# Kernel tuning notes

Measured on AMD Instinct MI355X. Metric: run time of the kernel, lower is better.

## Reference

```python
import jax, jax.numpy as jnp
import numpy as np

IGNORE_INDEX = -100
ALPHA = 1.0
TOPK = 20


def setup_inputs() -> dict:
    key = jax.random.key(0)
    k1, k2 = jax.random.split(key)
    N, V = 4096, 50257
    source = jax.random.normal(k1, (N, V), dtype=jnp.float32)
    target = jax.random.randint(k2, (N,), 0, V, dtype=jnp.int64)
    return {"source": source, "target": target}


def reference(source, target):
    s = source.astype(jnp.float32)  # [N, V]
    valid = target != IGNORE_INDEX  # [N]

    # per-token cross entropy, reduction='none' (0 at ignored positions)
    lse = jax.nn.logsumexp(s, axis=-1)  # [N]
    safe_tgt = jnp.where(valid, target, 0)
    tgt_logit = jnp.take_along_axis(s, safe_tgt[:, None], axis=-1)[:, 0]
    per_token_loss = jnp.where(valid, lse - tgt_logit, 0.0)

    # entropy-based adaptive weight over top-k logits (no grad in original)
    k = min(TOPK, s.shape[-1])
    topk_val, _ = jax.lax.top_k(s, k)  # [N, k]
    log_probs_topk = topk_val - jax.nn.logsumexp(topk_val, axis=-1, keepdims=True)
    entropy_approx = -(jnp.exp(log_probs_topk) * log_probs_topk).sum(axis=-1)
    adaptive_weight = jnp.power(entropy_approx / 3.0, ALPHA)
    adaptive_weight = jnp.where(valid, adaptive_weight, 0.0)
    adaptive_weight = jax.lax.stop_gradient(adaptive_weight)

    # reduction='mean' over valid tokens
    loss = (per_token_loss * adaptive_weight).sum() / valid.sum()
    return loss.astype(source.dtype)
```

## Files before the change

kernel.cpp:

```cpp
#include <hip/hip_runtime.h>
#include <stdint.h>

#define TOPK 20
#define BLK 256
#define CAP 4096
#define DELTA 2.0f
#define LSTRIDE 21
#define L2E 1.4426950408889634f
#define IGNORE_INDEX (-100)

__device__ __forceinline__ unsigned fkey(float x) {
  unsigned b = __float_as_uint(x);
  return (b & 0x80000000u) ? ~b : (b | 0x80000000u);
}
__device__ __forceinline__ float funkey(unsigned k) {
  unsigned b = (k & 0x80000000u) ? (k & 0x7FFFFFFFu) : ~k;
  return __uint_as_float(b);
}

struct LSE { float m; float l; };
__device__ __forceinline__ void lse_up(LSE& s, float x) {
  if (x > s.m) { s.l *= exp2f((s.m - x) * L2E); s.m = x; }
  s.l += exp2f((x - s.m) * L2E);
}

__device__ __forceinline__ void ins20(float (&tv)[TOPK], float c) {
  if (c > tv[TOPK - 1]) {
#pragma unroll
    for (int j = 0; j < TOPK; ++j) {
      float hi = fmaxf(tv[j], c);
      c = fminf(tv[j], c);
      tv[j] = hi;
    }
  }
}

__device__ __forceinline__ void merge2(const float* A, const float* B, float* O) {
  int i = 1, j = 1;
  float a = A[0], b = B[0];
#pragma unroll
  for (int k = 0; k < TOPK; ++k) {
    if (a >= b) { O[k] = a; a = A[i]; ++i; }
    else        { O[k] = b; b = B[j]; ++j; }
  }
}

__device__ float* merge64(int tid, float* bufA, float* bufB) {
  float* srcb = bufA;
  float* dstb = bufB;
  for (int s = 32; s >= 1; s >>= 1) {
    __syncthreads();
    if (tid < s) {
      merge2(srcb + tid * LSTRIDE, srcb + (tid + s) * LSTRIDE, dstb + tid * LSTRIDE);
      dstb[tid * LSTRIDE + TOPK] = -INFINITY;
    }
    float* t = srcb; srcb = dstb; dstb = t;
  }
  __syncthreads();
  return srcb;
}

__global__ __launch_bounds__(BLK) void eaft_ce_kernel(
    const float* __restrict__ src, const int* __restrict__ tgt,
    float* __restrict__ acc, int V) {
  __shared__ float s_cand[CAP];
  __shared__ float s_bufA[64 * LSTRIDE];
  __shared__ float s_bufB[64 * LSTRIDE];
  __shared__ float s_m[BLK];
  __shared__ float s_l[BLK];
  __shared__ unsigned s_maxkey;
  __shared__ int s_cnt;
  __shared__ int s_slow;

  const int tid = threadIdx.x;
  const int row = blockIdx.x;
  if (tid == 0) { s_maxkey = 0u; s_cnt = 0; s_slow = 0; }
  __syncthreads();

  const size_t rowbase = (size_t)row * (size_t)V;
  const float* arow = src + rowbase;
  const int mis = (int)(rowbase & 3);
  const int head = (4 - mis) & 3;
  const float4* vp = (const float4*)(arow + head);
  const int nvec = (V - head) >> 2;
  const int tail = V - head - (nvec << 2);

  LSE st; st.m = -INFINITY; st.l = 0.f;
  float lmax = -INFINITY;

  float4 pv = make_float4(-INFINITY, -INFINITY, -INFINITY, -INFINITY);
  if (tid < nvec) pv = vp[tid];
  float ex = -INFINITY;
  if (tid < head) ex = arow[tid];
  else if (tid >= 64 && tid < 64 + tail) ex = arow[head + (nvec << 2) + (tid - 64)];

  {
    float vals[5] = {pv.x, pv.y, pv.z, pv.w, ex};
#pragma unroll
    for (int q = 0; q < 5; ++q) {
      float x = vals[q];
      if (x != -INFINITY) {
        lse_up(st, x);
        if (x > lmax) { lmax = x; atomicMax(&s_maxkey, fkey(x)); }
      }
    }
  }
  __syncthreads();

  {
    float bm = funkey(*(volatile unsigned*)&s_maxkey);
    if (bm > lmax) lmax = bm;
    float T = bm - DELTA;
    float vals[5] = {pv.x, pv.y, pv.z, pv.w, ex};
#pragma unroll
    for (int q = 0; q < 5; ++q) {
      float x = vals[q];
      if (x >= T) {
        int p = atomicAdd(&s_cnt, 1);
        if (p < CAP) s_cand[p] = x;
      }
    }
  }

  for (int i = BLK + tid; i < nvec; i += BLK) {
    float4 x4 = vp[i];
    unsigned k = *(volatile unsigned*)&s_maxkey;
    float bm = funkey(k);
    if (bm > lmax) lmax = bm;
    float T = bm - DELTA;
    float vv[4] = {x4.x, x4.y, x4.z, x4.w};
#pragma unroll
    for (int q = 0; q < 4; ++q) {
      float x = vv[q];
      lse_up(st, x);
      if (x > lmax) { lmax = x; atomicMax(&s_maxkey, fkey(x)); }
      if (x >= T) {
        int p = atomicAdd(&s_cnt, 1);
        if (p < CAP) s_cand[p] = x;
      }
    }
  }

  s_m[tid] = st.m; s_l[tid] = st.l;
  __syncthreads();
  for (int s = BLK / 2; s > 0; s >>= 1) {
    if (tid < s) {
      float m1 = s_m[tid], l1 = s_l[tid];
      float m2 = s_m[tid + s], l2 = s_l[tid + s];
      float M = fmaxf(m1, m2);
      float w1 = (m1 > -INFINITY) ? l1 * exp2f((m1 - M) * L2E) : 0.f;
      float w2 = (m2 > -INFINITY) ? l2 * exp2f((m2 - M) * L2E) : 0.f;
      s_m[tid] = M; s_l[tid] = w1 + w2;
    }
    __syncthreads();
  }
  const float m_row = s_m[0];
  const float lse_row = m_row + logf(s_l[0]);

  const int cnt_raw = s_cnt;
  const int C = cnt_raw < CAP ? cnt_raw : CAP;
  if (tid < 64) {
    float tv[TOPK];
#pragma unroll
    for (int j = 0; j < TOPK; ++j) tv[j] = -INFINITY;
    for (int i = tid; i < C; i += 64) ins20(tv, s_cand[i]);
#pragma unroll
    for (int j = 0; j < TOPK; ++j) s_bufA[tid * LSTRIDE + j] = tv[j];
    s_bufA[tid * LSTRIDE + TOPK] = -INFINITY;
  }
  float* R = merge64(tid, s_bufA, s_bufB);

  if (tid == 0)
    s_slow = (cnt_raw > CAP || R[TOPK - 1] < m_row - DELTA) ? 1 : 0;
  __syncthreads();

  if (s_slow) {
    float tv[TOPK];
#pragma unroll
    for (int j = 0; j < TOPK; ++j) tv[j] = -INFINITY;
    for (int e = tid; e < V; e += BLK) ins20(tv, arow[e]);
    for (int r = 0; r < 4; ++r) {
      __syncthreads();
      if ((tid >> 6) == r) {
        int lane = tid & 63;
#pragma unroll
        for (int j = 0; j < TOPK; ++j) s_bufA[lane * LSTRIDE + j] = tv[j];
        s_bufA[lane * LSTRIDE + TOPK] = -INFINITY;
      }
      float* Rr = merge64(tid, s_bufA, s_bufB);
      if (tid == 0) {
#pragma unroll
        for (int j = 0; j < TOPK; ++j) s_cand[r * LSTRIDE + j] = Rr[j];
        s_cand[r * LSTRIDE + TOPK] = -INFINITY;
      }
      __syncthreads();
    }
    if (tid == 0) {
      merge2(s_cand + 0 * LSTRIDE, s_cand + 1 * LSTRIDE, s_bufA);
      s_bufA[TOPK] = -INFINITY;
      merge2(s_cand + 2 * LSTRIDE, s_cand + 3 * LSTRIDE, s_bufA + LSTRIDE);
      s_bufA[LSTRIDE + TOPK] = -INFINITY;
      merge2(s_bufA, s_bufA + LSTRIDE, s_bufB);
    }
  }
  __syncthreads();

  if (tid == 0) {
    const float* W = s_slow ? s_bufB : R;
    int t = tgt[row];
    if (t != IGNORE_INDEX) {
      float tl = arow[t];
      float loss = lse_row - tl;
      float m0 = W[0];
      float S1 = 0.f, Sv = 0.f;
#pragma unroll
      for (int k2 = 0; k2 < TOPK; ++k2) {
        float v = W[k2];
        float e = exp2f((v - m0) * L2E);
        S1 += e;
        Sv += v * e;
      }
      float ent = (m0 + logf(S1)) - Sv / S1;
      float w = ent * (1.0f / 3.0f);
      atomicAdd(&acc[0], w * loss);
      atomicAdd(&acc[1], 1.0f);
    }
  }
}

__global__ void finalize_kernel(const float* __restrict__ acc, float* __restrict__ out) {
  out[0] = acc[0] / acc[1];
}

extern "C" void kernel_launch(void* const* d_in, const int* in_sizes, int n_in,
                              void* d_out, int out_size, void* d_ws, size_t ws_size,
                              hipStream_t stream) {
  const float* src = (const float*)d_in[0];
  const int* tgt = (const int*)d_in[1];
  const int NV = in_sizes[0];
  const int n = in_sizes[1];
  const int V = NV / n;
  float* ws = (float*)d_ws;
  hipMemsetAsync(ws, 0, 2 * sizeof(float), stream);
  eaft_ce_kernel<<<n, BLK, 0, stream>>>(src, tgt, ws, V);
  finalize_kernel<<<1, 1, 0, stream>>>(ws, (float*)d_out);
}
```

Before: 1.191 ms.

## Use block-shared max for LSE, wave-shuffle reduction, nontemporal 2x-unrolled loads

Per-thread online-softmax rescaling is replaced by a shared running block max: after the first chunk, each thread accumulates exp(x - bm) and rescales only when the shared max grows. This removes a per-element compare-and-rescale. The shared-memory tree reduction becomes a wave-level shuffle reduction plus a 4-way final combine. The main loop is unrolled 2x with nontemporal vector loads, and the candidate buffer is halved to cut LDS use. Risks are more fallbacks to the slow path when candidates overflow, and cross-thread max-update races that are handled by the rescaling.

New measurement: 1.309 ms. 9.9% more time.

```diff
diff --git a/kernel.cpp b/kernel.cpp
--- a/kernel.cpp
+++ b/kernel.cpp
@@ -3,12 +3,14 @@
 
 #define TOPK 20
 #define BLK 256
-#define CAP 4096
+#define CAP 2048
 #define DELTA 2.0f
 #define LSTRIDE 21
 #define L2E 1.4426950408889634f
 #define IGNORE_INDEX (-100)
 
+typedef float f4v __attribute__((ext_vector_type(4)));
+
 __device__ __forceinline__ unsigned fkey(float x) {
   unsigned b = __float_as_uint(x);
   return (b & 0x80000000u) ? ~b : (b | 0x80000000u);
@@ -16,12 +18,6 @@
 __device__ __forceinline__ float funkey(unsigned k) {
   unsigned b = (k & 0x80000000u) ? (k & 0x7FFFFFFFu) : ~k;
   return __uint_as_float(b);
-}
-
-struct LSE { float m; float l; };
-__device__ __forceinline__ void lse_up(LSE& s, float x) {
-  if (x > s.m) { s.l *= exp2f((s.m - x) * L2E); s.m = x; }
-  s.l += exp2f((x - s.m) * L2E);
 }
 
 __device__ __forceinline__ void ins20(float (&tv)[TOPK], float c) {
@@ -66,8 +62,8 @@
   __shared__ float s_cand[CAP];
   __shared__ float s_bufA[64 * LSTRIDE];
   __shared__ float s_bufB[64 * LSTRIDE];
-  __shared__ float s_m[BLK];
-  __shared__ float s_l[BLK];
+  __shared__ float s_wm[4];
+  __shared__ float s_wl[4];
   __shared__ unsigned s_maxkey;
   __shared__ int s_cnt;
   __shared__ int s_slow;
@@ -79,83 +75,109 @@
 
   const size_t rowbase = (size_t)row * (size_t)V;
   const float* arow = src + rowbase;
-  const int mis = (int)(rowbase & 3);
-  const int head = (4 - mis) & 3;
-  const float4* vp = (const float4*)(arow + head);
+  const int head = (int)((4 - (rowbase & 3)) & 3);
+  const f4v* vp = (const f4v*)(arow + head);
   const int nvec = (V - head) >> 2;
   const int tail = V - head - (nvec << 2);
 
-  LSE st; st.m = -INFINITY; st.l = 0.f;
-  float lmax = -INFINITY;
-
-  float4 pv = make_float4(-INFINITY, -INFINITY, -INFINITY, -INFINITY);
-  if (tid < nvec) pv = vp[tid];
+  f4v pv = {-INFINITY, -INFINITY, -INFINITY, -INFINITY};
+  if (tid < nvec) pv = __builtin_nontemporal_load(vp + tid);
   float ex = -INFINITY;
   if (tid < head) ex = arow[tid];
   else if (tid >= 64 && tid < 64 + tail) ex = arow[head + (nvec << 2) + (tid - 64)];
 
+  float pmax = fmaxf(fmaxf(fmaxf(pv.x, pv.y), fmaxf(pv.z, pv.w)), ex);
+  if (pmax > -INFINITY) atomicMax(&s_maxkey, fkey(pmax));
+  __syncthreads();
+
+  float bm = funkey(s_maxkey);
+  float lmax = bm;
+  float cexp = -bm * L2E;
+  float l0 = 0.f, l1 = 0.f;
+
   {
+    float T = bm - DELTA;
     float vals[5] = {pv.x, pv.y, pv.z, pv.w, ex};
 #pragma unroll
     for (int q = 0; q < 5; ++q) {
       float x = vals[q];
-      if (x != -INFINITY) {
-        lse_up(st, x);
+      l0 += exp2f(fmaf(x, L2E, cexp));
+      if (x >= T) {
+        int p = atomicAdd(&s_cnt, 1);
+        if (p < CAP) s_cand[p] = x;
         if (x > lmax) { lmax = x; atomicMax(&s_maxkey, fkey(x)); }
       }
     }
   }
-  __syncthreads();
+
+  int i = BLK + tid;
+  for (; i + BLK < nvec; i += 2 * BLK) {
+    f4v a = __builtin_nontemporal_load(vp + i);
+    f4v b = __builtin_nontemporal_load(vp + i + BLK);
+    float nb = funkey(*(volatile unsigned*)&s_maxkey);
+    if (nb > bm) {
+      float r = exp2f((bm - nb) * L2E);
+      l0 *= r; l1 *= r;
+      bm = nb; cexp = -bm * L2E;
+      if (nb > lmax) lmax = nb;
+    }
+    float T = bm - DELTA;
+    float av[4] = {a.x, a.y, a.z, a.w};
+    float bv[4] = {b.x, b.y, b.z, b.w};
+#pragma unroll
+    for (int q = 0; q < 4; ++q) {
+      float x = av[q];
+      l0 += exp2f(fmaf(x, L2E, cexp));
+      if (x >= T) {
+        int p = atomicAdd(&s_cnt, 1);
+        if (p < CAP) s_cand[p] = x;
+        if (x > lmax) { lmax = x; atomicMax(&s_maxkey, fkey(x)); }
+      }
+      float y = bv[q];
+      l1 += exp2f(fmaf(y, L2E, cexp));
+      if (y >= T) {
+        int p = atomicAdd(&s_cnt, 1);
+        if (p < CAP) s_cand[p] = y;
+        if (y > lmax) { lmax = y; atomicMax(&s_maxkey, fkey(y)); }
+      }
+    }
+  }
+  if (i < nvec) {
+    f4v a = __builtin_nontemporal_load(vp + i);
+    float nb = funkey(*(volatile unsigned*)&s_maxkey);
+    if (nb > bm) {
+      float r = exp2f((bm - nb) * L2E);
+      l0 *= r; l1 *= r;
+      bm = nb; cexp = -bm * L2E;
+      if (nb > lmax) lmax = nb;
+    }
+    float T = bm - DELTA;
+    float av[4] = {a.x, a.y, a.z, a.w};
+#pragma unroll
+    for (int q = 0; q < 4; ++q) {
+      float x = av[q];
+      l0 += exp2f(fmaf(x, L2E, cexp));
+      if (x >= T) {
+        int p = atomicAdd(&s_cnt, 1);
+        if (p < CAP) s_cand[p] = x;
+        if (x > lmax) { lmax = x; atomicMax(&s_maxkey, fkey(x)); }
+      }
+    }
+  }
 
   {
-    float bm = funkey(*(volatile unsigned*)&s_maxkey);
-    if (bm > lmax) lmax = bm;
-    float T = bm - DELTA;
-    float vals[5] = {pv.x, pv.y, pv.z, pv.w, ex};
-#pragma unroll
-    for (int q = 0; q < 5; ++q) {
-      float x = vals[q];
-      if (x >= T) {
-        int p = atomicAdd(&s_cnt, 1);
-        if (p < CAP) s_cand[p] = x;
-      }
-    }
-  }
-
-  for (int i = BLK + tid; i < nvec; i += BLK) {
-    float4 x4 = vp[i];
-    unsigned k = *(volatile unsigned*)&s_maxkey;
-    float bm = funkey(k);
-    if (bm > lmax) lmax = bm;
-    float T = bm - DELTA;
-    float vv[4] = {x4.x, x4.y, x4.z, x4.w};
-#pragma unroll
-    for (int q = 0; q < 4; ++q) {
-      float x = vv[q];
-      lse_up(st, x);
-      if (x > lmax) { lmax = x; atomicMax(&s_maxkey, fkey(x)); }
-      if (x >= T) {
-        int p = atomicAdd(&s_cnt, 1);
-        if (p < CAP) s_cand[p] = x;
-      }
-    }
-  }
-
-  s_m[tid] = st.m; s_l[tid] = st.l;
-  __syncthreads();
-  for (int s = BLK / 2; s > 0; s >>= 1) {
-    if (tid < s) {
-      float m1 = s_m[tid], l1 = s_l[tid];
-      float m2 = s_m[tid + s], l2 = s_l[tid + s];
-      float M = fmaxf(m1, m2);
-      float w1 = (m1 > -INFINITY) ? l1 * exp2f((m1 - M) * L2E) : 0.f;
-      float w2 = (m2 > -INFINITY) ? l2 * exp2f((m2 - M) * L2E) : 0.f;
-      s_m[tid] = M; s_l[tid] = w1 + w2;
-    }
-    __syncthreads();
-  }
-  const float m_row = s_m[0];
-  const float lse_row = m_row + logf(s_l[0]);
+    float m = bm, l = l0 + l1;
+#pragma unroll
+    for (int off = 32; off > 0; off >>= 1) {
+      float om = __shfl_down(m, off);
+      float ol = __shfl_down(l, off);
+      float M = fmaxf(m, om);
+      l = l * exp2f((m - M) * L2E) + ol * exp2f((om - M) * L2E);
+      m = M;
+    }
+    if ((tid & 63) == 0) { s_wm[tid >> 6] = m; s_wl[tid >> 6] = l; }
+  }
+  __syncthreads();
 
   const int cnt_raw = s_cnt;
   const int C = cnt_raw < CAP ? cnt_raw : CAP;
@@ -163,15 +185,16 @@
     float tv[TOPK];
 #pragma unroll
     for (int j = 0; j < TOPK; ++j) tv[j] = -INFINITY;
-    for (int i = tid; i < C; i += 64) ins20(tv, s_cand[i]);
+    for (int k = tid; k < C; k += 64) ins20(tv, s_cand[k]);
 #pragma unroll
     for (int j = 0; j < TOPK; ++j) s_bufA[tid * LSTRIDE + j] = tv[j];
     s_bufA[tid * LSTRIDE + TOPK] = -INFINITY;
   }
   float* R = merge64(tid, s_bufA, s_bufB);
 
+  const float tmax = funkey(s_maxkey);
   if (tid == 0)
-    s_slow = (cnt_raw > CAP || R[TOPK - 1] < m_row - DELTA) ? 1 : 0;
+    s_slow = (cnt_raw > CAP || R[TOPK - 1] < tmax - DELTA) ? 1 : 0;
   __syncthreads();
 
   if (s_slow) {
@@ -209,6 +232,12 @@
     const float* W = s_slow ? s_bufB : R;
     int t = tgt[row];
     if (t != IGNORE_INDEX) {
+      float M = fmaxf(fmaxf(s_wm[0], s_wm[1]), fmaxf(s_wm[2], s_wm[3]));
+      float S = 0.f;
+#pragma unroll
+      for (int k = 0; k < 4; ++k) S += s_wl[k] * exp2f((s_wm[k] - M) * L2E);
+      const float lse_row = M + logf(S);
+
       float tl = arow[t];
       float loss = lse_row - tl;
       float m0 = W[0];
```
